# Performance work log

Hardware: AMD Instinct MI355X
Metric: run time of the kernel (lower is better)

Reference implementation:

```python
import jax, jax.numpy as jnp
import numpy as np
from jax import lax

B, T, D, U = 64, 512, 512, 1024


def setup_inputs() -> dict:
    key = jax.random.key(0)
    k1, k2, k3 = jax.random.split(key, 3)
    x = jax.random.normal(k1, (B, T, D), dtype=jnp.float32)
    Wx = jax.random.normal(k2, (D, 4 * U), dtype=jnp.float32) * (1.0 / np.sqrt(D))
    Wh = jax.random.normal(k3, (U, 4 * U), dtype=jnp.float32) * (1.0 / np.sqrt(U))
    # bias init: zeros(i), ones(f), zeros(c), zeros(o)
    b = jnp.concatenate([jnp.zeros((U,)), jnp.ones((U,)), jnp.zeros((2 * U,))]).astype(jnp.float32)
    return {"x": x, "Wx": Wx, "Wh": Wh, "b": b}


def reference(x, Wx, Wh, b):
    units = Wh.shape[0]
    batch = x.shape[0]
    # Precompute input projections for all timesteps: [B, T, 4U]
    xz = jnp.einsum('btd,dz->btz', x, Wx)

    def step(carry, zx_t):
        h, c = carry
        z = zx_t + h @ Wh + b            # [B, 4U]
        zi, zf, zg, zo = jnp.split(z, 4, axis=-1)
        i = jax.nn.sigmoid(zi)
        f = jax.nn.sigmoid(zf)
        c_new = f * c + i * jnp.tanh(zg)
        o = jax.nn.sigmoid(zo)
        h_new = o * jnp.tanh(c_new)
        return (h_new, c_new), None

    h0 = jnp.zeros((batch, units), dtype=x.dtype)
    c0 = jnp.zeros((batch, units), dtype=x.dtype)
    (h_last, c_last), _ = lax.scan(step, (h0, c0), jnp.swapaxes(xz, 0, 1))
    # return_sequence=False, return_states=False -> last hidden state
    return h_last
```

## Files before the change

### kernel.cpp

```cpp
#include <hip/hip_runtime.h>
#include <hip/hip_bf16.h>


#define T_STEPS 512
#define BATCH   64
#define DIM     512
#define UNITS   1024
#define ZCOLS   4096
#define MR      16
#define RING    64

typedef float        f32x4 __attribute__((ext_vector_type(4)));
typedef unsigned int u32x4 __attribute__((ext_vector_type(4)));

__device__ __forceinline__ f32x4 mfma16x16x32_bf16(u32x4 a, u32x4 b, f32x4 c) {
    asm("v_mfma_f32_16x16x32_bf16 %0, %1, %2, %0" : "+v"(c) : "v"(a), "v"(b));
    return c;
}

__device__ __forceinline__ unsigned short f2bf(float f) {
    union { float f; unsigned u; } v; v.f = f;
    unsigned r = v.u + 0x7fffu + ((v.u >> 16) & 1u);
    return (unsigned short)(r >> 16);
}

__device__ __forceinline__ float fsigmoid(float x) { return 1.0f / (1.0f + __expf(-x)); }
__device__ __forceinline__ float ftanh(float x)    { return 1.0f - 2.0f / (__expf(2.0f * x) + 1.0f); }

__device__ __forceinline__ u32x4 pack8(const float* __restrict__ p) {
    float4 f0 = reinterpret_cast<const float4*>(p)[0];
    float4 f1 = reinterpret_cast<const float4*>(p)[1];
    u32x4 r;
    r.x = (unsigned)f2bf(f0.x) | ((unsigned)f2bf(f0.y) << 16);
    r.y = (unsigned)f2bf(f0.z) | ((unsigned)f2bf(f0.w) << 16);
    r.z = (unsigned)f2bf(f1.x) | ((unsigned)f2bf(f1.y) << 16);
    r.w = (unsigned)f2bf(f1.z) | ((unsigned)f2bf(f1.w) << 16);
    return r;
}

#define LD4(d, base) \
    asm volatile("global_load_dwordx4 %0, %1, off sc0 sc1" : "=v"(d) : "v"(base));
#define LDW(d, base) \
    asm volatile("global_load_dword %0, %1, off sc0 sc1\n\ts_waitcnt vmcnt(0)" \
                 : "=v"(d) : "v"(base) : "memory");
#define STW(base, v) \
    asm volatile("global_store_dword %0, %1, off sc0 sc1" :: "v"(base), "v"(v) : "memory");
#define WAITV0 \
    asm volatile("s_waitcnt vmcnt(0)" ::: "memory"); \
    __builtin_amdgcn_sched_barrier(0);


__global__ void k_transpose_bf16(const float* __restrict__ in, unsigned short* __restrict__ out,
                                 int K, int N) {
    __shared__ float tile[32][33];
    int n0 = blockIdx.x * 32, k0 = blockIdx.y * 32;
    int tx = threadIdx.x, ty = threadIdx.y;
    tile[ty][tx] = in[(size_t)(k0 + ty) * N + n0 + tx];
    __syncthreads();
    out[(size_t)(n0 + ty) * K + k0 + tx] = f2bf(tile[tx][ty]);
}

__global__ void k_init(unsigned int* __restrict__ hbuf_u32,
                       unsigned int* __restrict__ hflags,
                       unsigned int* __restrict__ xzflags) {
    int i = blockIdx.x * blockDim.x + threadIdx.x;
    if (i < 65536) hbuf_u32[i] = 0u;
    else if (i < 65536 + 4096) hflags[i - 65536] = 0u;
    else if (i < 65536 + 4096 + 512) xzflags[i - 69632] = 0u;
}

__global__ __launch_bounds__(512, 1) void k_fused(
        const float* __restrict__ x,
        const unsigned short* __restrict__ WxT,
        const unsigned short* __restrict__ WhT,
        const float* __restrict__ bias,
        unsigned short* hbuf,
        float* __restrict__ out,
        unsigned int* hflags,
        unsigned int* xzflags,
        float* __restrict__ xzring) {
    __shared__ __align__(16) char smem[65536];
    const int tid  = threadIdx.x;
    const int lane = tid & 63;
    const int w    = tid >> 6;

    if (blockIdx.x < 128) {
        unsigned short* hs = (unsigned short*)smem;
        float* zb = (float*)(smem + 32768);
        const int ct  = w & 3;
        const int kh  = w >> 2;
        const int mg  = blockIdx.x >> 5;
        const int zbk = blockIdx.x & 31;
        const int r0  = mg * MR;
        const int u0  = zbk * 32;
        const int c16 = lane & 15;
        const int kl  = (lane >> 4) * 8;
        const int klb = (lane >> 4) * 16;

        u32x4 breg[2][16];
        #pragma unroll
        for (int n = 0; n < 2; ++n) {
            const unsigned short* wp =
                WhT + ((size_t)(ct * UNITS + u0 + n * 16 + c16)) * UNITS + kh * 512 + kl;
            #pragma unroll
            for (int kk = 0; kk < 16; ++kk) {
                breg[n][kk] = *reinterpret_cast<const u32x4*>(wp + kk * 32);
                asm volatile("" : "+v"(breg[n][kk]));
            }
        }

        const int ri = tid >> 5;
        const int ui = tid & 31;
        float creg = 0.0f;

        unsigned int* const myflag = hflags + (size_t)blockIdx.x * 32;
        const unsigned int* const gflags = hflags + (size_t)mg * 32 * 32;

        if (w == 0) {
            const unsigned int* fp = xzflags + (lane & 7);
            int iter = 0;
            for (;;) {
                unsigned v; LDW(v, fp)
                bool ok = (lane < 8) ? (v == 1u) : true;
                if (__all((int)ok)) break;
                if (++iter > (1 << 20)) break;
                __builtin_amdgcn_s_sleep(1);
            }
        }
        __syncthreads();

        for (int s = 0; s < T_STEPS; ++s) {
            const unsigned short* hrd = hbuf + (size_t)(s & 1) * (BATCH * UNITS);

            {
                u32x4 sv[4];
                #pragma unroll
                for (int j = 0; j < 4; ++j) {
                    int i = tid + j * 512;
                    int row = i >> 7, kc = i & 127;
                    const unsigned short* src = hrd + (size_t)(r0 + row) * UNITS + kc * 8;
                    LD4(sv[j], src)
                }
                WAITV0
                #pragma unroll
                for (int j = 0; j < 4; ++j) {
                    int i = tid + j * 512;
                    int row = i >> 7, kc = i & 127;
                    int lb = (row * 2048 + kc * 16) ^ ((row & 7) << 4);
                    *reinterpret_cast<u32x4*>(reinterpret_cast<char*>(hs) + lb) = sv[j];
                }
            }
            __syncthreads();

            float xv0, xv1, xv2, xv3;
            {
                const float* xp = xzring + ((size_t)(s & (RING - 1)) * BATCH + r0 + ri) * ZCOLS
                                  + u0 + ui;
                asm volatile("global_load_dword %0, %1, off sc0 sc1" : "=v"(xv0) : "v"(xp));
                asm volatile("global_load_dword %0, %1, off sc0 sc1" : "=v"(xv1) : "v"(xp + UNITS));
                asm volatile("global_load_dword %0, %1, off sc0 sc1" : "=v"(xv2) : "v"(xp + 2 * UNITS));
                asm volatile("global_load_dword %0, %1, off sc0 sc1" : "=v"(xv3) : "v"(xp + 3 * UNITS));
            }

            f32x4 acc0 = {0, 0, 0, 0}, acc1 = {0, 0, 0, 0};
            asm volatile("s_nop 1" : "+v"(acc0), "+v"(acc1));
            const char* abase = reinterpret_cast<const char*>(hs);
            const int axor = (c16 & 7) << 4;
            #pragma unroll
            for (int kk = 0; kk < 16; ++kk) {
                int lb = (c16 * 2048 + kh * 1024 + kk * 64 + klb) ^ axor;
                u32x4 a = *reinterpret_cast<const u32x4*>(abase + lb);
                acc0 = mfma16x16x32_bf16(a, breg[0][kk], acc0);
                acc1 = mfma16x16x32_bf16(a, breg[1][kk], acc1);
            }
            asm volatile("s_nop 7\n\ts_nop 7" : "+v"(acc0), "+v"(acc1));
            {
                const int rowq = (lane >> 4) * 4;
                #pragma unroll
                for (int r = 0; r < 4; ++r) {
                    zb[((kh * 16 + rowq + r)) * 132 + ct * 32 + c16]      = acc0[r];
                    zb[((kh * 16 + rowq + r)) * 132 + ct * 32 + 16 + c16] = acc1[r];
                }
            }
            __syncthreads();
            WAITV0

            {
                float zi = zb[ri * 132 + ui]      + zb[(16 + ri) * 132 + ui]      + xv0;
                float zf = zb[ri * 132 + 32 + ui] + zb[(16 + ri) * 132 + 32 + ui] + xv1;
                float zg = zb[ri * 132 + 64 + ui] + zb[(16 + ri) * 132 + 64 + ui] + xv2;
                float zo = zb[ri * 132 + 96 + ui] + zb[(16 + ri) * 132 + 96 + ui] + xv3;
                float ig = fsigmoid(zi), fg = fsigmoid(zf), gg = ftanh(zg), og = fsigmoid(zo);
                creg = fg * creg + ig * gg;
                float hn = og * ftanh(creg);
                unsigned hv = f2bf(hn);
                unsigned short* hwp = hbuf + (size_t)((s + 1) & 1) * (BATCH * UNITS)
                                      + (size_t)(r0 + ri) * UNITS + u0 + ui;
                asm volatile("global_store_short %0, %1, off sc0 sc1" :: "v"(hwp), "v"(hv) : "memory");
                if (s == T_STEPS - 1) out[(size_t)(r0 + ri) * UNITS + u0 + ui] = hn;
            }

            if (s < T_STEPS - 1) {
                WAITV0
                __syncthreads();
                if (tid == 0) {
                    STW(myflag, (unsigned)(s + 1))
                    asm volatile("s_waitcnt vmcnt(0)" ::: "memory");
                }
                if (w == 0) {
                    const unsigned tgtH = (unsigned)(s + 1);
                    const unsigned tgtX = (unsigned)(s + 2);
                    const unsigned int* fp = (lane < 32)
                        ? gflags + (size_t)lane * 32
                        : xzflags + (size_t)((s + 1) & (RING - 1)) * 8 + (lane & 7);
                    int iter = 0;
                    for (;;) {
                        unsigned v; LDW(v, fp)
                        bool ok = (lane < 32) ? (v >= tgtH)
                                  : ((lane < 40) ? (v == tgtX) : true);
                        if (__all((int)ok)) break;
                        if (++iter > (1 << 20)) break;
                        __builtin_amdgcn_s_sleep(1);
                    }
                }
                __syncthreads();
            }
        }
    } else {
        unsigned short* as_ = (unsigned short*)smem;
        const int p   = blockIdx.x - 128;
        const int bx  = p & 7;
        const int jt  = p >> 3;
        const int n0  = bx * 512 + w * 64;
        const int r16 = lane & 15;
        const int kl  = (lane >> 4) * 8;

        for (int k2 = 0; k2 < T_STEPS / 16; ++k2) {
            const int t = jt + 16 * k2;

            if (t >= RING) {
                if (w == 0) {
                    const unsigned need = (unsigned)(t - RING + 1);
                    int iter = 0;
                    for (;;) {
                        unsigned v0, v1;
                        LDW(v0, hflags + (size_t)lane * 32)
                        LDW(v1, hflags + (size_t)(lane + 64) * 32)
                        if (__all((int)(v0 >= need && v1 >= need))) break;
                        if (++iter > (1 << 20)) break;
                        __builtin_amdgcn_s_sleep(1);
                    }
                }
                __syncthreads();
            }

            for (int i = tid; i < 4096; i += 512) {
                int row = i >> 6, kc8 = i & 63;
                u32x4 v = pack8(x + ((size_t)row * T_STEPS + t) * DIM + kc8 * 8);
                int lb = (row * 1024 + kc8 * 16) ^ ((row & 7) << 4);
                *reinterpret_cast<u32x4*>(reinterpret_cast<char*>(as_) + lb) = v;
            }
            __syncthreads();

            const unsigned short* bp = WxT + (size_t)(n0 + r16) * DIM + kl;
            f32x4 acc[4][4] = {};
            asm volatile("s_nop 1" : "+v"(acc[0][0]), "+v"(acc[1][1]), "+v"(acc[2][2]), "+v"(acc[3][3]));
            #pragma unroll 2
            for (int kk = 0; kk < 16; ++kk) {
                u32x4 b0 = *reinterpret_cast<const u32x4*>(bp + kk * 32);
                u32x4 b1 = *reinterpret_cast<const u32x4*>(bp + 16 * DIM + kk * 32);
                u32x4 b2 = *reinterpret_cast<const u32x4*>(bp + 32 * DIM + kk * 32);
                u32x4 b3 = *reinterpret_cast<const u32x4*>(bp + 48 * DIM + kk * 32);
                u32x4 a[4];
                #pragma unroll
                for (int mt = 0; mt < 4; ++mt) {
                    int row = mt * 16 + r16;
                    int lb = (row * 1024 + (kk * 32 + kl) * 2) ^ ((row & 7) << 4);
                    a[mt] = *reinterpret_cast<const u32x4*>(reinterpret_cast<const char*>(as_) + lb);
                }
                #pragma unroll
                for (int mt = 0; mt < 4; ++mt) {
                    acc[mt][0] = mfma16x16x32_bf16(a[mt], b0, acc[mt][0]);
                    acc[mt][1] = mfma16x16x32_bf16(a[mt], b1, acc[mt][1]);
                    acc[mt][2] = mfma16x16x32_bf16(a[mt], b2, acc[mt][2]);
                    acc[mt][3] = mfma16x16x32_bf16(a[mt], b3, acc[mt][3]);
                }
            }
            asm volatile("s_nop 7\n\ts_nop 7" : "+v"(acc[0][0]), "+v"(acc[1][1]), "+v"(acc[2][2]), "+v"(acc[3][3]));

            {
                float* ringb = xzring + (size_t)(t & (RING - 1)) * BATCH * ZCOLS;
                const int rowq = (lane >> 4) * 4;
                #pragma unroll
                for (int nt = 0; nt < 4; ++nt) {
                    const int col = n0 + nt * 16 + r16;
                    const float bv = bias[col];
                    #pragma unroll
                    for (int mt = 0; mt < 4; ++mt) {
                        #pragma unroll
                        for (int r = 0; r < 4; ++r) {
                            float val = acc[mt][nt][r] + bv;
                            float* dst = ringb + (size_t)(mt * 16 + rowq + r) * ZCOLS + col;
                            asm volatile("global_store_dword %0, %1, off sc0 sc1"
                                         :: "v"(dst), "v"(val) : "memory");
                        }
                    }
                }
            }
            WAITV0
            __syncthreads();
            if (tid == 0) STW(xzflags + (size_t)(t & (RING - 1)) * 8 + bx, (unsigned)(t + 1))
            __syncthreads();
        }
    }
}


extern "C" void kernel_launch(void* const* d_in, const int* in_sizes, int n_in,
                              void* d_out, int out_size, void* d_ws, size_t ws_size,
                              hipStream_t stream) {
    const float* x    = (const float*)d_in[0];
    const float* Wx   = (const float*)d_in[1];
    const float* Wh   = (const float*)d_in[2];
    const float* bias = (const float*)d_in[3];

    char* ws = (char*)d_ws;
    unsigned short* WxT     = (unsigned short*)(ws);
    unsigned short* WhT     = (unsigned short*)(ws + (4u << 20));
    unsigned short* hbuf    = (unsigned short*)(ws + (12u << 20));
    unsigned int*   hflags  = (unsigned int*)(ws + (12u << 20) + (256u << 10));
    unsigned int*   xzflags = (unsigned int*)(ws + (12u << 20) + (272u << 10));
    float*          xzring  = (float*)(ws + (13u << 20));

    k_transpose_bf16<<<dim3(128, 16), dim3(32, 32), 0, stream>>>(Wx, WxT, 512, 4096);
    k_transpose_bf16<<<dim3(128, 32), dim3(32, 32), 0, stream>>>(Wh, WhT, 1024, 4096);
    k_init<<<160, 512, 0, stream>>>((unsigned int*)hbuf, hflags, xzflags);

    k_fused<<<256, 512, 0, stream>>>(x, WxT, WhT, bias, hbuf, (float*)d_out,
                                     hflags, xzflags, xzring);
}
```

Before: 1.643 ms.

## Tag hidden-state words with step number and pipeline two half-batches per block

Each hidden value is now stored as a 32-bit word holding the bf16 value plus a step tag in the upper half. Consumers spin directly on that data instead of per-block flags, which removes the separate flag store, the wait and the barrier from every step. Each block splits its 16 batch rows into two halves of 8 and alternates them, so loading one half's state overlaps with computing the other. Progress flags for the input-projection producers are written only every 8 steps. In exchange, hidden-state traffic doubles and the matmuls run at half row utilisation.

```diff
diff --git a/kernel.cpp b/kernel.cpp
--- a/kernel.cpp
+++ b/kernel.cpp
@@ -7,7 +7,6 @@
 #define DIM     512
 #define UNITS   1024
 #define ZCOLS   4096
-#define MR      16
 #define RING    64
 
 typedef float        f32x4 __attribute__((ext_vector_type(4)));
@@ -40,6 +39,8 @@
 
 #define LD4(d, base) \
     asm volatile("global_load_dwordx4 %0, %1, off sc0 sc1" : "=v"(d) : "v"(base));
+#define LDF(d, base) \
+    asm volatile("global_load_dword %0, %1, off sc0 sc1" : "=v"(d) : "v"(base));
 #define LDW(d, base) \
     asm volatile("global_load_dword %0, %1, off sc0 sc1\n\ts_waitcnt vmcnt(0)" \
                  : "=v"(d) : "v"(base) : "memory");
@@ -48,6 +49,12 @@
 #define WAITV0 \
     asm volatile("s_waitcnt vmcnt(0)" ::: "memory"); \
     __builtin_amdgcn_sched_barrier(0);
+#define WAITV1 \
+    asm volatile("s_waitcnt vmcnt(1)" ::: "memory"); \
+    __builtin_amdgcn_sched_barrier(0);
+#define WAITV4 \
+    asm volatile("s_waitcnt vmcnt(4)" ::: "memory"); \
+    __builtin_amdgcn_sched_barrier(0);
 
 
 __global__ void k_transpose_bf16(const float* __restrict__ in, unsigned short* __restrict__ out,
@@ -61,12 +68,12 @@
 }
 
 __global__ void k_init(unsigned int* __restrict__ hbuf_u32,
-                       unsigned int* __restrict__ hflags,
+                       unsigned int* __restrict__ prog,
                        unsigned int* __restrict__ xzflags) {
     int i = blockIdx.x * blockDim.x + threadIdx.x;
-    if (i < 65536) hbuf_u32[i] = 0u;
-    else if (i < 65536 + 4096) hflags[i - 65536] = 0u;
-    else if (i < 65536 + 4096 + 512) xzflags[i - 69632] = 0u;
+    if (i < 131072) hbuf_u32[i] = 0u;
+    else if (i < 135168) prog[i - 131072] = 0u;
+    else if (i < 135680) xzflags[i - 135168] = 0u;
 }
 
 __global__ __launch_bounds__(512, 1) void k_fused(
@@ -74,9 +81,9 @@
         const unsigned short* __restrict__ WxT,
         const unsigned short* __restrict__ WhT,
         const float* __restrict__ bias,
-        unsigned short* hbuf,
+        unsigned int* hbT,
         float* __restrict__ out,
-        unsigned int* hflags,
+        unsigned int* prog,
         unsigned int* xzflags,
         float* __restrict__ xzring) {
     __shared__ __align__(16) char smem[65536];
@@ -85,13 +92,16 @@
     const int w    = tid >> 6;
 
     if (blockIdx.x < 128) {
-        unsigned short* hs = (unsigned short*)smem;
-        float* zb = (float*)(smem + 32768);
+        char* hsA = smem;
+        char* hsB = smem + 16384;
+        float (*zb)[8][132] = (float (*)[8][132])(smem + 32768);
+
         const int ct  = w & 3;
         const int kh  = w >> 2;
         const int mg  = blockIdx.x >> 5;
         const int zbk = blockIdx.x & 31;
-        const int r0  = mg * MR;
+        const int rA0 = mg * 16;
+        const int rB0 = mg * 16 + 8;
         const int u0  = zbk * 32;
         const int c16 = lane & 15;
         const int kl  = (lane >> 4) * 8;
@@ -111,119 +121,212 @@
 
         const int ri = tid >> 5;
         const int ui = tid & 31;
-        float creg = 0.0f;
-
-        unsigned int* const myflag = hflags + (size_t)blockIdx.x * 32;
-        const unsigned int* const gflags = hflags + (size_t)mg * 32 * 32;
-
-        if (w == 0) {
-            const unsigned int* fp = xzflags + (lane & 7);
-            int iter = 0;
-            for (;;) {
-                unsigned v; LDW(v, fp)
-                bool ok = (lane < 8) ? (v == 1u) : true;
-                if (__all((int)ok)) break;
-                if (++iter > (1 << 20)) break;
-                __builtin_amdgcn_s_sleep(1);
-            }
+        float cregA = 0.0f, cregB = 0.0f;
+
+        int srow[4], scol[4];
+        #pragma unroll
+        for (int j = 0; j < 4; ++j) {
+            int c = tid + j * 512;
+            srow[j] = c >> 8;
+            scol[j] = (c & 255) * 4;
         }
-        __syncthreads();
+
+        unsigned int* const myprog = prog + (size_t)blockIdx.x * 32;
+
+        u32x4 av[4], bv[4];
+        #pragma unroll
+        for (int j = 0; j < 4; ++j) {
+            const unsigned int* p = hbT + (size_t)(rA0 + srow[j]) * UNITS + scol[j];
+            LD4(av[j], p)
+        }
 
         for (int s = 0; s < T_STEPS; ++s) {
-            const unsigned short* hrd = hbuf + (size_t)(s & 1) * (BATCH * UNITS);
+            const unsigned par  = (unsigned)(s & 1);
+            const unsigned parn = par ^ 1u;
+            unsigned int* const hb_r = hbT + (size_t)par * (BATCH * UNITS);
+            unsigned int* const hb_w = hbT + (size_t)parn * (BATCH * UNITS);
+            const int slot = s & (RING - 1);
+            const unsigned want = (unsigned)s;
+
+            if (s == 0) { WAITV0 }
+            else if (w < 4) { WAITV1 } else { WAITV0 }
 
             {
-                u32x4 sv[4];
+                int it = 0;
+                for (;;) {
+                    bool ok =
+                        (av[0].x >> 16) == want && (av[0].y >> 16) == want &&
+                        (av[0].z >> 16) == want && (av[0].w >> 16) == want &&
+                        (av[1].x >> 16) == want && (av[1].y >> 16) == want &&
+                        (av[1].z >> 16) == want && (av[1].w >> 16) == want &&
+                        (av[2].x >> 16) == want && (av[2].y >> 16) == want &&
+                        (av[2].z >> 16) == want && (av[2].w >> 16) == want &&
+                        (av[3].x >> 16) == want && (av[3].y >> 16) == want &&
+                        (av[3].z >> 16) == want && (av[3].w >> 16) == want;
+                    if (ok) break;
+                    if (++it > (1 << 15)) break;
+                    __builtin_amdgcn_s_sleep(1);
+                    #pragma unroll
+                    for (int j = 0; j < 4; ++j) {
+                        const unsigned int* p = hb_r + (size_t)(rA0 + srow[j]) * UNITS + scol[j];
+                        LD4(av[j], p)
+                    }
+                    WAITV0
+                }
+            }
+            #pragma unroll
+            for (int j = 0; j < 4; ++j) {
+                unsigned lo = (av[j].x & 0xffffu) | (av[j].y << 16);
+                unsigned hi = (av[j].z & 0xffffu) | (av[j].w << 16);
+                int lb = (srow[j] * 2048 + scol[j] * 2) ^ ((srow[j] & 7) << 4);
+                uint2 v2; v2.x = lo; v2.y = hi;
+                *reinterpret_cast<uint2*>(hsA + lb) = v2;
+            }
+            float xa0, xa1, xa2, xa3;
+            if (tid < 256) {
+                const float* xp = xzring + ((size_t)slot * BATCH + rA0 + ri) * ZCOLS + u0 + ui;
+                LDF(xa0, xp) LDF(xa1, xp + UNITS) LDF(xa2, xp + 2 * UNITS) LDF(xa3, xp + 3 * UNITS)
+            }
+            #pragma unroll
+            for (int j = 0; j < 4; ++j) {
+                const unsigned int* p = hb_r + (size_t)(rB0 + srow[j]) * UNITS + scol[j];
+                LD4(bv[j], p)
+            }
+            if (w == 0) {
+                const unsigned int* fp = xzflags + (size_t)slot * 8 + (lane & 7);
+                int it = 0;
+                for (;;) {
+                    unsigned v; LDW(v, fp)
+                    bool ok = (lane < 8) ? (v == (unsigned)(s + 1)) : true;
+                    if (__all((int)ok)) break;
+                    if (++it > (1 << 20)) break;
+                    __builtin_amdgcn_s_sleep(1);
+                }
+            }
+            __syncthreads();
+
+            {
+                f32x4 acc0 = {0, 0, 0, 0}, acc1 = {0, 0, 0, 0};
+                asm volatile("s_nop 1" : "+v"(acc0), "+v"(acc1));
+                const int arow = c16 & 7;
                 #pragma unroll
-                for (int j = 0; j < 4; ++j) {
-                    int i = tid + j * 512;
-                    int row = i >> 7, kc = i & 127;
-                    const unsigned short* src = hrd + (size_t)(r0 + row) * UNITS + kc * 8;
-                    LD4(sv[j], src)
-                }
-                WAITV0
+                for (int kk = 0; kk < 16; ++kk) {
+                    int lb = (arow * 2048 + kh * 1024 + kk * 64 + klb) ^ (arow << 4);
+                    u32x4 a = *reinterpret_cast<const u32x4*>(hsA + lb);
+                    acc0 = mfma16x16x32_bf16(a, breg[0][kk], acc0);
+                    acc1 = mfma16x16x32_bf16(a, breg[1][kk], acc1);
+                }
+                asm volatile("s_nop 7\n\ts_nop 7" : "+v"(acc0), "+v"(acc1));
+                if (lane < 32) {
+                    const int rowq = (lane >> 4) * 4;
+                    #pragma unroll
+                    for (int r = 0; r < 4; ++r) {
+                        zb[kh][rowq + r][ct * 32 + c16]      = acc0[r];
+                        zb[kh][rowq + r][ct * 32 + 16 + c16] = acc1[r];
+                    }
+                }
+            }
+            __syncthreads();
+
+            if (w < 4) { WAITV4 }
+            if (tid < 256) {
+                float zi = zb[0][ri][ui]      + zb[1][ri][ui]      + xa0;
+                float zf = zb[0][ri][32 + ui] + zb[1][ri][32 + ui] + xa1;
+                float zg = zb[0][ri][64 + ui] + zb[1][ri][64 + ui] + xa2;
+                float zo = zb[0][ri][96 + ui] + zb[1][ri][96 + ui] + xa3;
+                float ig = fsigmoid(zi), fg = fsigmoid(zf), gg = ftanh(zg), og = fsigmoid(zo);
+                cregA = fg * cregA + ig * gg;
+                float hn = og * ftanh(cregA);
+                unsigned hv = ((unsigned)(s + 1) << 16) | (unsigned)f2bf(hn);
+                unsigned int* hwp = hb_w + (size_t)(rA0 + ri) * UNITS + u0 + ui;
+                STW(hwp, hv)
+                if (s == T_STEPS - 1) out[(size_t)(rA0 + ri) * UNITS + u0 + ui] = hn;
+            }
+
+            if (w < 4) { WAITV1 } else { WAITV0 }
+            {
+                int it = 0;
+                for (;;) {
+                    bool ok =
+                        (bv[0].x >> 16) == want && (bv[0].y >> 16) == want &&
+                        (bv[0].z >> 16) == want && (bv[0].w >> 16) == want &&
+                        (bv[1].x >> 16) == want && (bv[1].y >> 16) == want &&
+                        (bv[1].z >> 16) == want && (bv[1].w >> 16) == want &&
+                        (bv[2].x >> 16) == want && (bv[2].y >> 16) == want &&
+                        (bv[2].z >> 16) == want && (bv[2].w >> 16) == want &&
+                        (bv[3].x >> 16) == want && (bv[3].y >> 16) == want &&
+                        (bv[3].z >> 16) == want && (bv[3].w >> 16) == want;
+                    if (ok) break;
+                    if (++it > (1 << 15)) break;
+                    __builtin_amdgcn_s_sleep(1);
+                    #pragma unroll
+                    for (int j = 0; j < 4; ++j) {
+                        const unsigned int* p = hb_r + (size_t)(rB0 + srow[j]) * UNITS + scol[j];
+                        LD4(bv[j], p)
+                    }
+                    WAITV0
+                }
+            }
+            #pragma unroll
+            for (int j = 0; j < 4; ++j) {
+                unsigned lo = (bv[j].x & 0xffffu) | (bv[j].y << 16);
+                unsigned hi = (bv[j].z & 0xffffu) | (bv[j].w << 16);
+                int lb = (srow[j] * 2048 + scol[j] * 2) ^ ((srow[j] & 7) << 4);
+                uint2 v2; v2.x = lo; v2.y = hi;
+                *reinterpret_cast<uint2*>(hsB + lb) = v2;
+            }
+            float xb0, xb1, xb2, xb3;
+            if (tid < 256) {
+                const float* xp = xzring + ((size_t)slot * BATCH + rB0 + ri) * ZCOLS + u0 + ui;
+                LDF(xb0, xp) LDF(xb1, xp + UNITS) LDF(xb2, xp + 2 * UNITS) LDF(xb3, xp + 3 * UNITS)
+            }
+            #pragma unroll
+            for (int j = 0; j < 4; ++j) {
+                const unsigned int* p = hb_w + (size_t)(rA0 + srow[j]) * UNITS + scol[j];
+                LD4(av[j], p)
+            }
+            __syncthreads();
+
+            {
+                f32x4 acc0 = {0, 0, 0, 0}, acc1 = {0, 0, 0, 0};
+                asm volatile("s_nop 1" : "+v"(acc0), "+v"(acc1));
+                const int arow = c16 & 7;
                 #pragma unroll
-                for (int j = 0; j < 4; ++j) {
-                    int i = tid + j * 512;
-                    int row = i >> 7, kc = i & 127;
-                    int lb = (row * 2048 + kc * 16) ^ ((row & 7) << 4);
-                    *reinterpret_cast<u32x4*>(reinterpret_cast<char*>(hs) + lb) = sv[j];
-                }
-            }
-            __syncthreads();
-
-            float xv0, xv1, xv2, xv3;
-            {
-                const float* xp = xzring + ((size_t)(s & (RING - 1)) * BATCH + r0 + ri) * ZCOLS
-                                  + u0 + ui;
-                asm volatile("global_load_dword %0, %1, off sc0 sc1" : "=v"(xv0) : "v"(xp));
-                asm volatile("global_load_dword %0, %1, off sc0 sc1" : "=v"(xv1) : "v"(xp + UNITS));
-                asm volatile("global_load_dword %0, %1, off sc0 sc1" : "=v"(xv2) : "v"(xp + 2 * UNITS));
-                asm volatile("global_load_dword %0, %1, off sc0 sc1" : "=v"(xv3) : "v"(xp + 3 * UNITS));
-            }
-
-            f32x4 acc0 = {0, 0, 0, 0}, acc1 = {0, 0, 0, 0};
-            asm volatile("s_nop 1" : "+v"(acc0), "+v"(acc1));
-            const char* abase = reinterpret_cast<const char*>(hs);
-            const int axor = (c16 & 7) << 4;
-            #pragma unroll
-            for (int kk = 0; kk < 16; ++kk) {
-                int lb = (c16 * 2048 + kh * 1024 + kk * 64 + klb) ^ axor;
-                u32x4 a = *reinterpret_cast<const u32x4*>(abase + lb);
-                acc0 = mfma16x16x32_bf16(a, breg[0][kk], acc0);
-                acc1 = mfma16x16x32_bf16(a, breg[1][kk], acc1);
-            }
-            asm volatile("s_nop 7\n\ts_nop 7" : "+v"(acc0), "+v"(acc1));
-            {
-                const int rowq = (lane >> 4) * 4;
-                #pragma unroll
-                for (int r = 0; r < 4; ++r) {
-                    zb[((kh * 16 + rowq + r)) * 132 + ct * 32 + c16]      = acc0[r];
-                    zb[((kh * 16 + rowq + r)) * 132 + ct * 32 + 16 + c16] = acc1[r];
-                }
-            }
-            __syncthreads();
-            WAITV0
-
-            {
-                float zi = zb[ri * 132 + ui]      + zb[(16 + ri) * 132 + ui]      + xv0;
-                float zf = zb[ri * 132 + 32 + ui] + zb[(16 + ri) * 132 + 32 + ui] + xv1;
-                float zg = zb[ri * 132 + 64 + ui] + zb[(16 + ri) * 132 + 64 + ui] + xv2;
-                float zo = zb[ri * 132 + 96 + ui] + zb[(16 + ri) * 132 + 96 + ui] + xv3;
+                for (int kk = 0; kk < 16; ++kk) {
+                    int lb = (arow * 2048 + kh * 1024 + kk * 64 + klb) ^ (arow << 4);
+                    u32x4 a = *reinterpret_cast<const u32x4*>(hsB + lb);
+                    acc0 = mfma16x16x32_bf16(a, breg[0][kk], acc0);
+                    acc1 = mfma16x16x32_bf16(a, breg[1][kk], acc1);
+                }
+                asm volatile("s_nop 7\n\ts_nop 7" : "+v"(acc0), "+v"(acc1));
+                if (lane < 32) {
+                    const int rowq = (lane >> 4) * 4;
+                    #pragma unroll
+                    for (int r = 0; r < 4; ++r) {
+                        zb[kh][rowq + r][ct * 32 + c16]      = acc0[r];
+                        zb[kh][rowq + r][ct * 32 + 16 + c16] = acc1[r];
+                    }
+                }
+            }
+            __syncthreads();
+
+            if (w < 4) { WAITV4 }
+            if (tid < 256) {
+                float zi = zb[0][ri][ui]      + zb[1][ri][ui]      + xb0;
+                float zf = zb[0][ri][32 + ui] + zb[1][ri][32 + ui] + xb1;
+                float zg = zb[0][ri][64 + ui] + zb[1][ri][64 + ui] + xb2;
+                float zo = zb[0][ri][96 + ui] + zb[1][ri][96 + ui] + xb3;
                 float ig = fsigmoid(zi), fg = fsigmoid(zf), gg = ftanh(zg), og = fsigmoid(zo);
-                creg = fg * creg + ig * gg;
-                float hn = og * ftanh(creg);
-                unsigned hv = f2bf(hn);
-                unsigned short* hwp = hbuf + (size_t)((s + 1) & 1) * (BATCH * UNITS)
-                                      + (size_t)(r0 + ri) * UNITS + u0 + ui;
-                asm volatile("global_store_short %0, %1, off sc0 sc1" :: "v"(hwp), "v"(hv) : "memory");
-                if (s == T_STEPS - 1) out[(size_t)(r0 + ri) * UNITS + u0 + ui] = hn;
-            }
-
-            if (s < T_STEPS - 1) {
-                WAITV0
-                __syncthreads();
-                if (tid == 0) {
-                    STW(myflag, (unsigned)(s + 1))
-                    asm volatile("s_waitcnt vmcnt(0)" ::: "memory");
-                }
-                if (w == 0) {
-                    const unsigned tgtH = (unsigned)(s + 1);
-                    const unsigned tgtX = (unsigned)(s + 2);
-                    const unsigned int* fp = (lane < 32)
-                        ? gflags + (size_t)lane * 32
-                        : xzflags + (size_t)((s + 1) & (RING - 1)) * 8 + (lane & 7);
-                    int iter = 0;
-                    for (;;) {
-                        unsigned v; LDW(v, fp)
-                        bool ok = (lane < 32) ? (v >= tgtH)
-                                  : ((lane < 40) ? (v == tgtX) : true);
-                        if (__all((int)ok)) break;
-                        if (++iter > (1 << 20)) break;
-                        __builtin_amdgcn_s_sleep(1);
-                    }
-                }
-                __syncthreads();
+                cregB = fg * cregB + ig * gg;
+                float hn = og * ftanh(cregB);
+                unsigned hv = ((unsigned)(s + 1) << 16) | (unsigned)f2bf(hn);
+                unsigned int* hwp = hb_w + (size_t)(rB0 + ri) * UNITS + u0 + ui;
+                STW(hwp, hv)
+                if (s == T_STEPS - 1) out[(size_t)(rB0 + ri) * UNITS + u0 + ui] = hn;
+            }
+
+            if ((((s + 1) & 7) == 0) && tid == 0) {
+                STW(myprog, (unsigned)(s + 1))
             }
         }
     } else {
@@ -244,8 +347,8 @@
                     int iter = 0;
                     for (;;) {
                         unsigned v0, v1;
-                        LDW(v0, hflags + (size_t)lane * 32)
-                        LDW(v1, hflags + (size_t)(lane + 64) * 32)
+                        LDW(v0, prog + (size_t)lane * 32)
+                        LDW(v1, prog + (size_t)(lane + 64) * 32)
                         if (__all((int)(v0 >= need && v1 >= need))) break;
                         if (++iter > (1 << 20)) break;
                         __builtin_amdgcn_s_sleep(1);
@@ -327,15 +430,15 @@
     char* ws = (char*)d_ws;
     unsigned short* WxT     = (unsigned short*)(ws);
     unsigned short* WhT     = (unsigned short*)(ws + (4u << 20));
-    unsigned short* hbuf    = (unsigned short*)(ws + (12u << 20));
-    unsigned int*   hflags  = (unsigned int*)(ws + (12u << 20) + (256u << 10));
-    unsigned int*   xzflags = (unsigned int*)(ws + (12u << 20) + (272u << 10));
+    unsigned int*   hbT     = (unsigned int*)(ws + (12u << 20));
+    unsigned int*   prog    = (unsigned int*)(ws + (12u << 20) + (512u << 10));
+    unsigned int*   xzflags = (unsigned int*)(ws + (12u << 20) + (528u << 10));
     float*          xzring  = (float*)(ws + (13u << 20));
 
     k_transpose_bf16<<<dim3(128, 16), dim3(32, 32), 0, stream>>>(Wx, WxT, 512, 4096);
     k_transpose_bf16<<<dim3(128, 32), dim3(32, 32), 0, stream>>>(Wh, WhT, 1024, 4096);
-    k_init<<<160, 512, 0, stream>>>((unsigned int*)hbuf, hflags, xzflags);
-
-    k_fused<<<256, 512, 0, stream>>>(x, WxT, WhT, bias, hbuf, (float*)d_out,
-                                     hflags, xzflags, xzring);
-}
+    k_init<<<512, 512, 0, stream>>>(hbT, prog, xzflags);
+
+    k_fused<<<256, 512, 0, stream>>>(x, WxT, WhT, bias, hbT, (float*)d_out,
+                                     prog, xzflags, xzring);
+}
```

Result: slower. 2.028 ms (+23.4%).

## Interleave gate columns in Wh and do the full K per wave

Applied to the files above, without the earlier changes.

Wh is repacked so the four gate columns of each unit sit next to each other. Each wave now covers the full K=1024 reduction for 16 interleaved gate columns, keeping 32 B fragments in registers, instead of splitting K across wave halves. The gate values are regrouped per lane with two xor-shuffle stages, which removes the LDS z-buffer round trip and one __syncthreads per timestep. The cost is twice the register footprint for B fragments and a longer serial MFMA chain per wave, split into two accumulators.

```diff
diff --git a/kernel.cpp b/kernel.cpp
--- a/kernel.cpp
+++ b/kernel.cpp
@@ -7,7 +7,6 @@
 #define DIM     512
 #define UNITS   1024
 #define ZCOLS   4096
-#define MR      16
 #define RING    64
 
 typedef float        f32x4 __attribute__((ext_vector_type(4)));
@@ -40,11 +39,15 @@
 
 #define LD4(d, base) \
     asm volatile("global_load_dwordx4 %0, %1, off sc0 sc1" : "=v"(d) : "v"(base));
+#define LDF(d, base) \
+    asm volatile("global_load_dword %0, %1, off sc0 sc1" : "=v"(d) : "v"(base));
 #define LDW(d, base) \
     asm volatile("global_load_dword %0, %1, off sc0 sc1\n\ts_waitcnt vmcnt(0)" \
                  : "=v"(d) : "v"(base) : "memory");
 #define STW(base, v) \
     asm volatile("global_store_dword %0, %1, off sc0 sc1" :: "v"(base), "v"(v) : "memory");
+#define STH(base, v) \
+    asm volatile("global_store_short %0, %1, off sc0 sc1" :: "v"(base), "v"(v) : "memory");
 #define WAITV0 \
     asm volatile("s_waitcnt vmcnt(0)" ::: "memory"); \
     __builtin_amdgcn_sched_barrier(0);
@@ -60,6 +63,17 @@
     out[(size_t)(n0 + ty) * K + k0 + tx] = f2bf(tile[tx][ty]);
 }
 
+__global__ void k_transpose_whp(const float* __restrict__ in, unsigned short* __restrict__ out) {
+    __shared__ float tile[32][33];
+    int n0 = blockIdx.x * 32, k0 = blockIdx.y * 32;
+    int tx = threadIdx.x, ty = threadIdx.y;
+    tile[ty][tx] = in[(size_t)(k0 + ty) * ZCOLS + n0 + tx];
+    __syncthreads();
+    int c = n0 + ty;
+    int r = ((c & 1023) << 2) | (c >> 10);
+    out[(size_t)r * UNITS + k0 + tx] = f2bf(tile[tx][ty]);
+}
+
 __global__ void k_init(unsigned int* __restrict__ hbuf_u32,
                        unsigned int* __restrict__ hflags,
                        unsigned int* __restrict__ xzflags) {
@@ -72,7 +86,7 @@
 __global__ __launch_bounds__(512, 1) void k_fused(
         const float* __restrict__ x,
         const unsigned short* __restrict__ WxT,
-        const unsigned short* __restrict__ WhT,
+        const unsigned short* __restrict__ WhP,
         const float* __restrict__ bias,
         unsigned short* hbuf,
         float* __restrict__ out,
@@ -85,32 +99,28 @@
     const int w    = tid >> 6;
 
     if (blockIdx.x < 128) {
-        unsigned short* hs = (unsigned short*)smem;
-        float* zb = (float*)(smem + 32768);
-        const int ct  = w & 3;
-        const int kh  = w >> 2;
+        char* hs = smem;
         const int mg  = blockIdx.x >> 5;
         const int zbk = blockIdx.x & 31;
-        const int r0  = mg * MR;
+        const int r0  = mg * 16;
         const int u0  = zbk * 32;
         const int c16 = lane & 15;
         const int kl  = (lane >> 4) * 8;
         const int klb = (lane >> 4) * 16;
 
-        u32x4 breg[2][16];
-        #pragma unroll
-        for (int n = 0; n < 2; ++n) {
+        u32x4 breg[32];
+        {
             const unsigned short* wp =
-                WhT + ((size_t)(ct * UNITS + u0 + n * 16 + c16)) * UNITS + kh * 512 + kl;
+                WhP + ((size_t)(zbk * 128 + w * 16 + c16)) * UNITS + kl;
             #pragma unroll
-            for (int kk = 0; kk < 16; ++kk) {
-                breg[n][kk] = *reinterpret_cast<const u32x4*>(wp + kk * 32);
-                asm volatile("" : "+v"(breg[n][kk]));
+            for (int kk = 0; kk < 32; ++kk) {
+                breg[kk] = *reinterpret_cast<const u32x4*>(wp + kk * 32);
+                asm volatile("" : "+v"(breg[kk]));
             }
         }
 
-        const int ri = tid >> 5;
-        const int ui = tid & 31;
+        const int row_l  = r0 + 4 * (lane >> 4) + (lane & 3);
+        const int unit_l = u0 + w * 4 + ((lane >> 2) & 3);
         float creg = 0.0f;
 
         unsigned int* const myflag = hflags + (size_t)blockIdx.x * 32;
@@ -131,6 +141,7 @@
 
         for (int s = 0; s < T_STEPS; ++s) {
             const unsigned short* hrd = hbuf + (size_t)(s & 1) * (BATCH * UNITS);
+            const int slot = s & (RING - 1);
 
             {
                 u32x4 sv[4];
@@ -147,57 +158,59 @@
                     int i = tid + j * 512;
                     int row = i >> 7, kc = i & 127;
                     int lb = (row * 2048 + kc * 16) ^ ((row & 7) << 4);
-                    *reinterpret_cast<u32x4*>(reinterpret_cast<char*>(hs) + lb) = sv[j];
+                    *reinterpret_cast<u32x4*>(hs + lb) = sv[j];
                 }
             }
             __syncthreads();
 
-            float xv0, xv1, xv2, xv3;
-            {
-                const float* xp = xzring + ((size_t)(s & (RING - 1)) * BATCH + r0 + ri) * ZCOLS
-                                  + u0 + ui;
-                asm volatile("global_load_dword %0, %1, off sc0 sc1" : "=v"(xv0) : "v"(xp));
-                asm volatile("global_load_dword %0, %1, off sc0 sc1" : "=v"(xv1) : "v"(xp + UNITS));
-                asm volatile("global_load_dword %0, %1, off sc0 sc1" : "=v"(xv2) : "v"(xp + 2 * UNITS));
-                asm volatile("global_load_dword %0, %1, off sc0 sc1" : "=v"(xv3) : "v"(xp + 3 * UNITS));
-            }
-
-            f32x4 acc0 = {0, 0, 0, 0}, acc1 = {0, 0, 0, 0};
-            asm volatile("s_nop 1" : "+v"(acc0), "+v"(acc1));
-            const char* abase = reinterpret_cast<const char*>(hs);
-            const int axor = (c16 & 7) << 4;
+            float x0, x1, x2, x3;
+            {
+                const float* xp = xzring + ((size_t)slot * BATCH + row_l) * ZCOLS + unit_l;
+                LDF(x0, xp) LDF(x1, xp + UNITS) LDF(x2, xp + 2 * UNITS) LDF(x3, xp + 3 * UNITS)
+            }
+
+            f32x4 ae = {0, 0, 0, 0}, ao = {0, 0, 0, 0};
+            asm volatile("s_nop 1" : "+v"(ae), "+v"(ao));
+            const int axorb = (c16 & 7) << 4;
             #pragma unroll
-            for (int kk = 0; kk < 16; ++kk) {
-                int lb = (c16 * 2048 + kh * 1024 + kk * 64 + klb) ^ axor;
-                u32x4 a = *reinterpret_cast<const u32x4*>(abase + lb);
-                acc0 = mfma16x16x32_bf16(a, breg[0][kk], acc0);
-                acc1 = mfma16x16x32_bf16(a, breg[1][kk], acc1);
-            }
-            asm volatile("s_nop 7\n\ts_nop 7" : "+v"(acc0), "+v"(acc1));
-            {
-                const int rowq = (lane >> 4) * 4;
-                #pragma unroll
-                for (int r = 0; r < 4; ++r) {
-                    zb[((kh * 16 + rowq + r)) * 132 + ct * 32 + c16]      = acc0[r];
-                    zb[((kh * 16 + rowq + r)) * 132 + ct * 32 + 16 + c16] = acc1[r];
-                }
-            }
-            __syncthreads();
+            for (int k2 = 0; k2 < 16; ++k2) {
+                int lb0 = (c16 * 2048 + (2 * k2) * 64 + klb) ^ axorb;
+                int lb1 = (c16 * 2048 + (2 * k2 + 1) * 64 + klb) ^ axorb;
+                u32x4 a0 = *reinterpret_cast<const u32x4*>(hs + lb0);
+                u32x4 a1 = *reinterpret_cast<const u32x4*>(hs + lb1);
+                ae = mfma16x16x32_bf16(a0, breg[2 * k2], ae);
+                ao = mfma16x16x32_bf16(a1, breg[2 * k2 + 1], ao);
+            }
+            asm volatile("s_nop 7\n\ts_nop 7" : "+v"(ae), "+v"(ao));
+
+            float v0, v1, v2, v3;
+            {
+                f32x4 zv = ae + ao;
+                v0 = zv[0]; v1 = zv[1]; v2 = zv[2]; v3 = zv[3];
+                float sa = (lane & 1) ? v0 : v1;
+                float sb = (lane & 1) ? v2 : v3;
+                float ra = __shfl_xor(sa, 1, 64);
+                float rb = __shfl_xor(sb, 1, 64);
+                if (lane & 1) { v0 = ra; v2 = rb; } else { v1 = ra; v3 = rb; }
+                float sc = (lane & 2) ? v0 : v2;
+                float sd = (lane & 2) ? v1 : v3;
+                float rc = __shfl_xor(sc, 2, 64);
+                float rd = __shfl_xor(sd, 2, 64);
+                if (lane & 2) { v0 = rc; v1 = rd; } else { v2 = rc; v3 = rd; }
+            }
+
             WAITV0
 
             {
-                float zi = zb[ri * 132 + ui]      + zb[(16 + ri) * 132 + ui]      + xv0;
-                float zf = zb[ri * 132 + 32 + ui] + zb[(16 + ri) * 132 + 32 + ui] + xv1;
-                float zg = zb[ri * 132 + 64 + ui] + zb[(16 + ri) * 132 + 64 + ui] + xv2;
-                float zo = zb[ri * 132 + 96 + ui] + zb[(16 + ri) * 132 + 96 + ui] + xv3;
+                float zi = v0 + x0, zf = v1 + x1, zg = v2 + x2, zo = v3 + x3;
                 float ig = fsigmoid(zi), fg = fsigmoid(zf), gg = ftanh(zg), og = fsigmoid(zo);
                 creg = fg * creg + ig * gg;
                 float hn = og * ftanh(creg);
                 unsigned hv = f2bf(hn);
                 unsigned short* hwp = hbuf + (size_t)((s + 1) & 1) * (BATCH * UNITS)
-                                      + (size_t)(r0 + ri) * UNITS + u0 + ui;
-                asm volatile("global_store_short %0, %1, off sc0 sc1" :: "v"(hwp), "v"(hv) : "memory");
-                if (s == T_STEPS - 1) out[(size_t)(r0 + ri) * UNITS + u0 + ui] = hn;
+                                      + (size_t)row_l * UNITS + unit_l;
+                STH(hwp, hv)
+                if (s == T_STEPS - 1) out[(size_t)row_l * UNITS + unit_l] = hn;
             }
 
             if (s < T_STEPS - 1) {
@@ -326,16 +339,16 @@
 
     char* ws = (char*)d_ws;
     unsigned short* WxT     = (unsigned short*)(ws);
-    unsigned short* WhT     = (unsigned short*)(ws + (4u << 20));
+    unsigned short* WhP     = (unsigned short*)(ws + (4u << 20));
     unsigned short* hbuf    = (unsigned short*)(ws + (12u << 20));
     unsigned int*   hflags  = (unsigned int*)(ws + (12u << 20) + (256u << 10));
     unsigned int*   xzflags = (unsigned int*)(ws + (12u << 20) + (272u << 10));
     float*          xzring  = (float*)(ws + (13u << 20));
 
     k_transpose_bf16<<<dim3(128, 16), dim3(32, 32), 0, stream>>>(Wx, WxT, 512, 4096);
-    k_transpose_bf16<<<dim3(128, 32), dim3(32, 32), 0, stream>>>(Wh, WhT, 1024, 4096);
+    k_transpose_whp<<<dim3(128, 32), dim3(32, 32), 0, stream>>>(Wh, WhP);
     k_init<<<160, 512, 0, stream>>>((unsigned int*)hbuf, hflags, xzflags);
 
-    k_fused<<<256, 512, 0, stream>>>(x, WxT, WhT, bias, hbuf, (float*)d_out,
+    k_fused<<<256, 512, 0, stream>>>(x, WxT, WhP, bias, hbuf, (float*)d_out,
                                      hflags, xzflags, xzring);
 }
```

After: 1.800 ms. 1.1x slower.
